# Kernel tuning notes

Measured on AMD Instinct MI355X. Metric: run time of the kernel, lower is better.

The kernel has to match this reference:

```python
import jax, jax.numpy as jnp
import numpy as np

N, E = 40000, 640000          # nodes, edges (avg degree 16)
IN_N, IN_E = 8 + 768, 2       # in_dim_node + in_dim_text, in_dim_edge
H, OUT, NC, L = 128, 128, 5, 2
EPS_BN, EPS_DEN = 1e-5, 1e-6


def setup_inputs() -> dict:
    key = jax.random.key(0)
    ks = jax.random.split(key, 16)
    w = lambda k, shape: jax.random.normal(k, shape, jnp.float32) * 0.05
    return {
        "node_feat": jax.random.normal(ks[0], (N, IN_N), jnp.float32),
        "edge_feat": jax.random.normal(ks[1], (E, IN_E), jnp.float32),
        "src": jax.random.randint(ks[2], (E,), 0, N),
        "dst": jax.random.randint(ks[3], (E,), 0, N),
        "enc_nw": w(ks[4], (IN_N, H)), "enc_nb": jnp.zeros((H,), jnp.float32),
        "enc_ew": w(ks[5], (IN_E, H)), "enc_eb": jnp.zeros((H,), jnp.float32),
        # per layer: 5 linears (order A, B, C, D, E)
        "lin_w": w(ks[6], (L, 5, H, H)), "lin_b": jnp.zeros((L, 5, H), jnp.float32),
        "bnh_g": jnp.ones((L, H), jnp.float32), "bnh_b": jnp.zeros((L, H), jnp.float32),
        "bne_g": jnp.ones((L, H), jnp.float32), "bne_b": jnp.zeros((L, H), jnp.float32),
        "mlp_w1": w(ks[7], (H, OUT)), "mlp_b1": jnp.zeros((OUT,), jnp.float32),
        "mlp_w2": w(ks[8], (OUT, NC)), "mlp_b2": jnp.zeros((NC,), jnp.float32),
    }


def _bn(x, g, b):
    # training-mode BatchNorm1d: batch stats, biased variance, eps=1e-5
    m = jnp.mean(x, axis=0)
    v = jnp.var(x, axis=0)
    return (x - m) * jax.lax.rsqrt(v + EPS_BN) * g + b


def reference(node_feat, edge_feat, src, dst, enc_nw, enc_nb, enc_ew, enc_eb,
              lin_w, lin_b, bnh_g, bnh_b, bne_g, bne_b,
              mlp_w1, mlp_b1, mlp_w2, mlp_b2):
    n = node_feat.shape[0]
    h = node_feat @ enc_nw + enc_nb          # [N, H]
    e = edge_feat @ enc_ew + enc_eb          # [E, H]
    for l in range(L):
        Ah = h @ lin_w[l, 0] + lin_b[l, 0]
        Bh = h @ lin_w[l, 1] + lin_b[l, 1]
        Ce = e @ lin_w[l, 2] + lin_b[l, 2]
        Dh = h @ lin_w[l, 3] + lin_b[l, 3]
        Eh = h @ lin_w[l, 4] + lin_b[l, 4]
        e_new = Ce + Dh[src] + Eh[dst]       # [E, H] edge gate logits
        sigma = jax.nn.sigmoid(e_new)
        num = jax.ops.segment_sum(sigma * Bh[src], dst, num_segments=n)
        den = jax.ops.segment_sum(sigma, dst, num_segments=n)
        h_new = Ah + num / (den + EPS_DEN)
        h = jax.nn.relu(_bn(h_new, bnh_g[l], bnh_b[l]))
        e = jax.nn.relu(_bn(e_new, bne_g[l], bne_b[l]))
    # MLP readout per node (dropout p=0 -> identity)
    logits = jax.nn.relu(h @ mlp_w1 + mlp_b1) @ mlp_w2 + mlp_b2
    return logits
```

## Files before the change

### kernel.cpp

```cpp
#include <hip/hip_runtime.h>
#include <math.h>

#define NN 40000
#define NE 640000
#define KIN 776
#define HH 128
#define NCLS 5

typedef __attribute__((ext_vector_type(8))) short bf16x8;
typedef __attribute__((ext_vector_type(4))) short bf16x4;
typedef __attribute__((ext_vector_type(4))) float f32x4;

__device__ __forceinline__ float bf2f(short u) {
    return __uint_as_float(((unsigned)(unsigned short)u) << 16);
}
__device__ __forceinline__ short f2bf(float f) {
    unsigned u = __float_as_uint(f);
    u += 0x7fffu + ((u >> 16) & 1u);
    return (short)(u >> 16);
}

enum { A_F32 = 0, A_BF16 = 1, A_BN = 2, A_BNF32 = 3 };

template<int AMODE, int NSTEP, bool TAIL8, bool GATHER, bool RELUOUT, bool CBF16>
__global__ __launch_bounds__(256)
void mfma_gemm(const float* __restrict__ Af, const short* __restrict__ Ab,
               const short* __restrict__ Wp, const float* __restrict__ bias,
               float* __restrict__ Cf, short* __restrict__ Cb,
               const float* __restrict__ bnp,
               const short* __restrict__ Dh, const short* __restrict__ Eh,
               const int* __restrict__ src, const int* __restrict__ dstv,
               int K)
{
    const int lane = threadIdx.x & 63;
    const int wave = threadIdx.x >> 6;
    const int q = lane >> 4;
    const int c16 = lane & 15;
    const int row = blockIdx.x * 64 + wave * 16 + c16;

    f32x4 acc[8];
#pragma unroll
    for (int n = 0; n < 8; ++n) acc[n] = (f32x4){0.f, 0.f, 0.f, 0.f};

    for (int kt = 0; kt < NSTEP; ++kt) {
        bf16x8 afrag;
        const int kbase = kt * 32 + q * 8;
        if (AMODE == A_BF16) {
            afrag = *(const bf16x8*)(Ab + (size_t)row * K + kbase);
        } else if (AMODE == A_F32) {
            if (!TAIL8 || kt < NSTEP - 1 || q == 0) {
                const float* p = Af + (size_t)row * K + kbase;
                const float4 x = *(const float4*)p;
                const float4 y = *(const float4*)(p + 4);
                afrag[0] = f2bf(x.x); afrag[1] = f2bf(x.y);
                afrag[2] = f2bf(x.z); afrag[3] = f2bf(x.w);
                afrag[4] = f2bf(y.x); afrag[5] = f2bf(y.y);
                afrag[6] = f2bf(y.z); afrag[7] = f2bf(y.w);
            } else {
#pragma unroll
                for (int j = 0; j < 8; ++j) afrag[j] = 0;
            }
        } else if (AMODE == A_BN) {
            const bf16x8 raw = *(const bf16x8*)(Ab + (size_t)row * K + kbase);
            const float4 s0 = *(const float4*)(bnp + kbase);
            const float4 s1 = *(const float4*)(bnp + kbase + 4);
            const float4 t0 = *(const float4*)(bnp + HH + kbase);
            const float4 t1 = *(const float4*)(bnp + HH + kbase + 4);
            const float scv[8] = {s0.x, s0.y, s0.z, s0.w, s1.x, s1.y, s1.z, s1.w};
            const float shv[8] = {t0.x, t0.y, t0.z, t0.w, t1.x, t1.y, t1.z, t1.w};
#pragma unroll
            for (int j = 0; j < 8; ++j)
                afrag[j] = f2bf(fmaxf(fmaf(bf2f(raw[j]), scv[j], shv[j]), 0.f));
        } else {
            const float* p = Af + (size_t)row * K + kbase;
            const float4 x = *(const float4*)p;
            const float4 y = *(const float4*)(p + 4);
            const float4 s0 = *(const float4*)(bnp + kbase);
            const float4 s1 = *(const float4*)(bnp + kbase + 4);
            const float4 t0 = *(const float4*)(bnp + HH + kbase);
            const float4 t1 = *(const float4*)(bnp + HH + kbase + 4);
            const float xv[8] = {x.x, x.y, x.z, x.w, y.x, y.y, y.z, y.w};
            const float scv[8] = {s0.x, s0.y, s0.z, s0.w, s1.x, s1.y, s1.z, s1.w};
            const float shv[8] = {t0.x, t0.y, t0.z, t0.w, t1.x, t1.y, t1.z, t1.w};
#pragma unroll
            for (int j = 0; j < 8; ++j)
                afrag[j] = f2bf(fmaxf(fmaf(xv[j], scv[j], shv[j]), 0.f));
        }
        const int kb = kt * 4 + q;
#pragma unroll
        for (int n = 0; n < 8; ++n) {
            const bf16x8 wfrag =
                *(const bf16x8*)(Wp + (size_t)kb * 1024 + (n * 16 + c16) * 8);
            acc[n] = __builtin_amdgcn_mfma_f32_16x16x32_bf16(wfrag, afrag, acc[n], 0, 0, 0);
        }
    }

    int sI = 0, dI = 0;
    if (GATHER) { sI = src[row]; dI = dstv[row]; }
#pragma unroll
    for (int n = 0; n < 8; ++n) {
        const int col = n * 16 + q * 4;
        const float4 b4 = *(const float4*)(bias + col);
        float v[4] = {acc[n][0] + b4.x, acc[n][1] + b4.y,
                      acc[n][2] + b4.z, acc[n][3] + b4.w};
        if (GATHER) {
            const bf16x4 dh = *(const bf16x4*)(Dh + (size_t)sI * HH + col);
            const bf16x4 eh = *(const bf16x4*)(Eh + (size_t)dI * HH + col);
#pragma unroll
            for (int j = 0; j < 4; ++j) v[j] += bf2f(dh[j]) + bf2f(eh[j]);
        }
        if (RELUOUT) {
#pragma unroll
            for (int j = 0; j < 4; ++j) v[j] = fmaxf(v[j], 0.f);
        }
        if (CBF16) {
            bf16x4 o;
#pragma unroll
            for (int j = 0; j < 4; ++j) o[j] = f2bf(v[j]);
            *(bf16x4*)(Cb + (size_t)row * HH + col) = o;
        } else {
            *(float4*)(Cf + (size_t)row * HH + col) = make_float4(v[0], v[1], v[2], v[3]);
        }
    }
}

template<bool ABN>
__global__ __launch_bounds__(256, 2)
void fused4_k(const short* __restrict__ hb, const float* __restrict__ hf,
              const float* __restrict__ bnp,
              const short* __restrict__ w0, const short* __restrict__ w1,
              const short* __restrict__ w2, const short* __restrict__ w3,
              const float* __restrict__ b0, const float* __restrict__ b1,
              const float* __restrict__ b2, const float* __restrict__ b3,
              float* __restrict__ Ah, short* __restrict__ Bh,
              short* __restrict__ Dh, short* __restrict__ Eh)
{
    const int lane = threadIdx.x & 63;
    const int wave = threadIdx.x >> 6;
    const int q = lane >> 4;
    const int c16 = lane & 15;
    const int row = blockIdx.x * 64 + wave * 16 + c16;

    f32x4 acc[4][8];
#pragma unroll
    for (int t = 0; t < 4; ++t)
#pragma unroll
        for (int n = 0; n < 8; ++n) acc[t][n] = (f32x4){0.f, 0.f, 0.f, 0.f};

    const short* const ws[4] = {w0, w1, w2, w3};
#pragma unroll
    for (int kt = 0; kt < 4; ++kt) {
        const int kbase = kt * 32 + q * 8;
        bf16x8 afrag;
        if (!ABN) {
            afrag = *(const bf16x8*)(hb + (size_t)row * HH + kbase);
        } else {
            const float* p = hf + (size_t)row * HH + kbase;
            const float4 x = *(const float4*)p;
            const float4 y = *(const float4*)(p + 4);
            const float4 s0 = *(const float4*)(bnp + kbase);
            const float4 s1 = *(const float4*)(bnp + kbase + 4);
            const float4 t0 = *(const float4*)(bnp + HH + kbase);
            const float4 t1 = *(const float4*)(bnp + HH + kbase + 4);
            const float xv[8] = {x.x, x.y, x.z, x.w, y.x, y.y, y.z, y.w};
            const float scv[8] = {s0.x, s0.y, s0.z, s0.w, s1.x, s1.y, s1.z, s1.w};
            const float shv[8] = {t0.x, t0.y, t0.z, t0.w, t1.x, t1.y, t1.z, t1.w};
#pragma unroll
            for (int j = 0; j < 8; ++j)
                afrag[j] = f2bf(fmaxf(fmaf(xv[j], scv[j], shv[j]), 0.f));
        }
        const int kb = kt * 4 + q;
#pragma unroll
        for (int t = 0; t < 4; ++t)
#pragma unroll
            for (int n = 0; n < 8; ++n) {
                const bf16x8 wfrag =
                    *(const bf16x8*)(ws[t] + (size_t)kb * 1024 + (n * 16 + c16) * 8);
                acc[t][n] = __builtin_amdgcn_mfma_f32_16x16x32_bf16(wfrag, afrag, acc[t][n], 0, 0, 0);
            }
    }

    const float* const bs[4] = {b0, b1, b2, b3};
#pragma unroll
    for (int t = 0; t < 4; ++t) {
#pragma unroll
        for (int n = 0; n < 8; ++n) {
            const int col = n * 16 + q * 4;
            const float4 b4 = *(const float4*)(bs[t] + col);
            const float v[4] = {acc[t][n][0] + b4.x, acc[t][n][1] + b4.y,
                                acc[t][n][2] + b4.z, acc[t][n][3] + b4.w};
            if (t == 0) {
                *(float4*)(Ah + (size_t)row * HH + col) = make_float4(v[0], v[1], v[2], v[3]);
            } else {
                bf16x4 o;
#pragma unroll
                for (int j = 0; j < 4; ++j) o[j] = f2bf(v[j]);
                short* dstp = (t == 1) ? Bh : ((t == 2) ? Dh : Eh);
                *(bf16x4*)(dstp + (size_t)row * HH + col) = o;
            }
        }
    }
}

__global__ __launch_bounds__(256)
void prepack_k(const float* __restrict__ enc_nw, const float* __restrict__ lin_w,
               const float* __restrict__ mlp_w1, short* __restrict__ wp)
{
    const int t = blockIdx.x * 256 + threadIdx.x;
    if (t >= 260 * 128) return;
    const int kbg = t >> 7, col = t & 127;
    const int kb0[11]  = {0, 100, 116, 132, 148, 164, 180, 196, 212, 228, 244};
    const int psel[11] = {0, 1, 1, 1, 1, 1, 1, 1, 1, 1, 2};
    const int soff[11] = {0, 0 * 16384, 1 * 16384, 3 * 16384, 4 * 16384,
                          5 * 16384, 6 * 16384, 7 * 16384, 8 * 16384, 9 * 16384, 0};
    const int Ksrc[11] = {KIN, 128, 128, 128, 128, 128, 128, 128, 128, 128, 128};
    int e = 10;
    while (e > 0 && kbg < kb0[e]) --e;
    const float* base = (psel[e] == 0) ? enc_nw : ((psel[e] == 1) ? lin_w : mlp_w1);
    const int kbl = kbg - kb0[e];
    bf16x8 o;
#pragma unroll
    for (int j = 0; j < 8; ++j) {
        const int k = kbl * 8 + j;
        const float v = (k < Ksrc[e]) ? base[(size_t)soff[e] + (size_t)k * HH + col] : 0.f;
        o[j] = f2bf(v);
    }
    *(bf16x8*)(wp + (size_t)kbg * 1024 + col * 8) = o;
}

__global__ void gpre_k(const float* __restrict__ enc_ew, const float* __restrict__ enc_eb,
                       const float* __restrict__ Wc, const float* __restrict__ bc,
                       float* __restrict__ G)
{
    const int c = threadIdx.x;
    float a0 = 0.f, a1 = 0.f, ab = 0.f;
    for (int k = 0; k < HH; ++k) {
        const float w = Wc[k * HH + c];
        a0 = fmaf(enc_ew[k], w, a0);
        a1 = fmaf(enc_ew[HH + k], w, a1);
        ab = fmaf(enc_eb[k], w, ab);
    }
    G[c] = a0; G[HH + c] = a1; G[2 * HH + c] = ab + bc[c];
}

__global__ __launch_bounds__(256)
void edge1_k(const float* __restrict__ ef, const int* __restrict__ eidx,
             const int* __restrict__ src_s, const int* __restrict__ dst_s,
             const float* __restrict__ G,
             const short* __restrict__ Dh, const short* __restrict__ Eh,
             short* __restrict__ enew, float* __restrict__ pbuf)
{
    const int tid = threadIdx.x;
    const int er = tid >> 4, cg = tid & 15;
    const int col = cg * 8;
    const float4 g00 = *(const float4*)(G + col);
    const float4 g01 = *(const float4*)(G + col + 4);
    const float4 g10 = *(const float4*)(G + HH + col);
    const float4 g11 = *(const float4*)(G + HH + col + 4);
    const float4 gb0 = *(const float4*)(G + 2 * HH + col);
    const float4 gb1 = *(const float4*)(G + 2 * HH + col + 4);
    const float G0v[8] = {g00.x, g00.y, g00.z, g00.w, g01.x, g01.y, g01.z, g01.w};
    const float G1v[8] = {g10.x, g10.y, g10.z, g10.w, g11.x, g11.y, g11.z, g11.w};
    const float GBv[8] = {gb0.x, gb0.y, gb0.z, gb0.w, gb1.x, gb1.y, gb1.z, gb1.w};
    float sa[8] = {}, qa[8] = {};
    for (int it = 0; it < 16; ++it) {
        const int i = blockIdx.x * 256 + it * 16 + er;
        const int e = eidx[i];
        const float f0 = ef[(size_t)e * 2];
        const float f1 = ef[(size_t)e * 2 + 1];
        const int s = src_s[i], d = dst_s[i];
        const bf16x8 dh = *(const bf16x8*)(Dh + (size_t)s * HH + col);
        const bf16x8 eh = *(const bf16x8*)(Eh + (size_t)d * HH + col);
        bf16x8 o;
#pragma unroll
        for (int j = 0; j < 8; ++j) {
            const float v = fmaf(f0, G0v[j], fmaf(f1, G1v[j], GBv[j]))
                            + bf2f(dh[j]) + bf2f(eh[j]);
            sa[j] += v; qa[j] += v * v;
            o[j] = f2bf(v);
        }
        *(bf16x8*)(enew + (size_t)i * HH + col) = o;
    }
    __shared__ float sred[16][136];
    const int slot = (blockIdx.x & 63) * 256;
#pragma unroll
    for (int j = 0; j < 8; ++j) sred[er][col + j] = sa[j];
    __syncthreads();
    for (int s2 = 8; s2 > 0; s2 >>= 1) {
        if (er < s2)
#pragma unroll
            for (int j = 0; j < 8; ++j) sred[er][col + j] += sred[er + s2][col + j];
        __syncthreads();
    }
    if (er == 0)
#pragma unroll
        for (int j = 0; j < 8; ++j) atomicAdd(pbuf + slot + col + j, sred[0][col + j]);
    __syncthreads();
#pragma unroll
    for (int j = 0; j < 8; ++j) sred[er][col + j] = qa[j];
    __syncthreads();
    for (int s2 = 8; s2 > 0; s2 >>= 1) {
        if (er < s2)
#pragma unroll
            for (int j = 0; j < 8; ++j) sred[er][col + j] += sred[er + s2][col + j];
        __syncthreads();
    }
    if (er == 0)
#pragma unroll
        for (int j = 0; j < 8; ++j) atomicAdd(pbuf + slot + 128 + col + j, sred[0][col + j]);
}

__global__ __launch_bounds__(256)
void hist_k(const int* __restrict__ dst, int* __restrict__ cnt)
{
    const int e = blockIdx.x * 256 + threadIdx.x;
    if (e < NE) atomicAdd(cnt + dst[e], 1);
}

__global__ __launch_bounds__(1024)
void scan_k(const int* __restrict__ cnt, int* __restrict__ rowptr, int* __restrict__ wr)
{
    __shared__ int s[1024];
    const int t = threadIdx.x;
    const int base = t * 40;
    int sum = 0;
    for (int i = 0; i < 40; ++i) {
        const int idx = base + i;
        if (idx < NN) sum += cnt[idx];
    }
    s[t] = sum;
    __syncthreads();
    for (int off = 1; off < 1024; off <<= 1) {
        const int v = (t >= off) ? s[t - off] : 0;
        __syncthreads();
        s[t] += v;
        __syncthreads();
    }
    int run = (t == 0) ? 0 : s[t - 1];
    for (int i = 0; i < 40; ++i) {
        const int idx = base + i;
        if (idx < NN) {
            rowptr[idx] = run;
            wr[idx] = run;
            run += cnt[idx];
        }
    }
    if (t == 1023) rowptr[NN] = s[1023];
}

__global__ __launch_bounds__(256)
void scatter_k2(const int* __restrict__ dst, const int* __restrict__ src,
                int* __restrict__ wr, int* __restrict__ eidx,
                int* __restrict__ src_s, int* __restrict__ dst_s)
{
    const int e = blockIdx.x * 256 + threadIdx.x;
    if (e < NE) {
        const int d = dst[e];
        const int p = atomicAdd(wr + d, 1);
        eidx[p] = e;
        src_s[p] = src[e];
        dst_s[p] = d;
    }
}

__global__ __launch_bounds__(128)
void seg_reduce8(const short* __restrict__ enew, const int* __restrict__ rowptr,
                 const int* __restrict__ src_s, const short* __restrict__ Bh,
                 const float* __restrict__ Ah, float* __restrict__ hnew,
                 float* __restrict__ pbuf)
{
    const int c = threadIdx.x;
    const int nb = blockIdx.x * 8;
    float sa = 0.f, qa = 0.f;
    for (int nn = 0; nn < 8; ++nn) {
        const int n = nb + nn;
        const int k0 = rowptr[n], k1 = rowptr[n + 1];
        float num = 0.f, den = 0.f;
        for (int k = k0; k < k1; ++k) {
            const float x = bf2f(enew[(size_t)k * HH + c]);
            const float sg = 1.f / (1.f + __expf(-x));
            const float bh = bf2f(Bh[(size_t)src_s[k] * HH + c]);
            den += sg;
            num = fmaf(sg, bh, num);
        }
        const size_t idx = (size_t)n * HH + c;
        const float x = Ah[idx] + num / (den + 1e-6f);
        hnew[idx] = x;
        sa += x; qa += x * x;
    }
    const int slot = (blockIdx.x & 63) * 256;
    atomicAdd(pbuf + slot + c, sa);
    atomicAdd(pbuf + slot + 128 + c, qa);
}

__global__ void make_bnp2(const float* __restrict__ pbuf, const float* __restrict__ g,
                          const float* __restrict__ b, float cntInv,
                          float* __restrict__ out)
{
    const int c = threadIdx.x;
    float s = 0.f, q = 0.f;
    for (int i = 0; i < 64; ++i) {
        s += pbuf[i * 256 + c];
        q += pbuf[i * 256 + 128 + c];
    }
    const float m = s * cntInv;
    const float var = q * cntInv - m * m;
    const float rs = rsqrtf(var + 1e-5f);
    const float sc = g[c] * rs;
    out[c] = sc;
    out[128 + c] = b[c] - m * sc;
}

__global__ __launch_bounds__(256)
void readout2(const short* __restrict__ z, const float* __restrict__ w2,
              const float* __restrict__ b2, float* __restrict__ out)
{
    const int idx = blockIdx.x * 256 + threadIdx.x;
    if (idx >= NN * NCLS) return;
    const int n = idx / NCLS, j = idx - n * NCLS;
    float acc = b2[j];
    const short* zr = z + (size_t)n * HH;
    for (int kk = 0; kk < 16; ++kk) {
        const bf16x8 zv = *(const bf16x8*)(zr + kk * 8);
#pragma unroll
        for (int j8 = 0; j8 < 8; ++j8)
            acc = fmaf(bf2f(zv[j8]), w2[(kk * 8 + j8) * NCLS + j], acc);
    }
    out[idx] = acc;
}

extern "C" void kernel_launch(void* const* d_in, const int* in_sizes, int n_in,
                              void* d_out, int out_size, void* d_ws, size_t ws_size,
                              hipStream_t stream)
{
    const float* node_feat = (const float*)d_in[0];
    const float* edge_feat = (const float*)d_in[1];
    const int*   src       = (const int*)d_in[2];
    const int*   dst       = (const int*)d_in[3];
    const float* enc_nw    = (const float*)d_in[4];
    const float* enc_nb    = (const float*)d_in[5];
    const float* enc_ew    = (const float*)d_in[6];
    const float* enc_eb    = (const float*)d_in[7];
    const float* lin_w     = (const float*)d_in[8];
    const float* lin_b     = (const float*)d_in[9];
    const float* bnh_g     = (const float*)d_in[10];
    const float* bnh_b     = (const float*)d_in[11];
    const float* bne_g     = (const float*)d_in[12];
    const float* bne_b     = (const float*)d_in[13];
    const float* mlp_w1    = (const float*)d_in[14];
    const float* mlp_b1    = (const float*)d_in[15];
    const float* mlp_w2    = (const float*)d_in[16];
    const float* mlp_b2    = (const float*)d_in[17];
    float* out = (float*)d_out;

    char* base = (char*)d_ws;
    size_t off = 0;
    auto alloc = [&](size_t bytes) -> void* {
        void* p = base + off;
        off = (off + bytes + 255) & ~(size_t)255;
        return p;
    };
    const size_t NH = (size_t)NN * HH;
    float* hnew  = (float*)alloc(NH * 4);
    float* Ah    = (float*)alloc(NH * 4);
    short* h0    = (short*)alloc(NH * 2);
    short* Bh    = (short*)alloc(NH * 2);
    short* Dh    = (short*)alloc(NH * 2);
    short* Eh    = (short*)alloc(NH * 2);
    short* z     = (short*)alloc(NH * 2);
    short* enew  = (short*)alloc((size_t)NE * HH * 2);
    short* wpack = (short*)alloc((size_t)260 * 1024 * 2);
    float* G     = (float*)alloc(384 * 4);
    float* bnpe  = (float*)alloc(256 * 4);
    float* bnph  = (float*)alloc(256 * 4);
    float* pbe   = (float*)alloc(16384 * 4);
    float* pbh0  = (float*)alloc(16384 * 4);
    float* pbh1  = (float*)alloc(16384 * 4);
    int* cnt     = (int*)alloc(NN * 4);
    int* rowptr  = (int*)alloc((NN + 1) * 4);
    int* wr      = (int*)alloc(NN * 4);
    int* eidx    = (int*)alloc((size_t)NE * 4);
    int* src_s   = (int*)alloc((size_t)NE * 4);
    int* dst_s   = (int*)alloc((size_t)NE * 4);

    const dim3 blk(256);

    hipMemsetAsync(cnt, 0, NN * 4, stream);
    hipMemsetAsync(pbe, 0, 3 * 16384 * 4, stream);
    hist_k<<<2500, blk, 0, stream>>>(dst, cnt);
    scan_k<<<1, 1024, 0, stream>>>(cnt, rowptr, wr);
    scatter_k2<<<2500, blk, 0, stream>>>(dst, src, wr, eidx, src_s, dst_s);
    prepack_k<<<130, blk, 0, stream>>>(enc_nw, lin_w, mlp_w1, wpack);
    gpre_k<<<1, 128, 0, stream>>>(enc_ew, enc_eb, lin_w + 2 * 16384, lin_b + 2 * HH, G);

    mfma_gemm<A_F32, 25, true, false, false, true><<<625, blk, 0, stream>>>(
        node_feat, nullptr, wpack, enc_nb, nullptr, h0,
        nullptr, nullptr, nullptr, nullptr, nullptr, KIN);

    {
        const float* Bv = lin_b;
        fused4_k<false><<<625, blk, 0, stream>>>(
            h0, nullptr, nullptr,
            wpack + (size_t)100 * 1024, wpack + (size_t)116 * 1024,
            wpack + (size_t)132 * 1024, wpack + (size_t)148 * 1024,
            Bv + 0 * HH, Bv + 1 * HH, Bv + 3 * HH, Bv + 4 * HH,
            Ah, Bh, Dh, Eh);
        edge1_k<<<2500, blk, 0, stream>>>(edge_feat, eidx, src_s, dst_s, G,
                                          Dh, Eh, enew, pbe);
        make_bnp2<<<1, 128, 0, stream>>>(pbe, bne_g, bne_b, 1.f / NE, bnpe);
        seg_reduce8<<<5000, 128, 0, stream>>>(enew, rowptr, src_s, Bh, Ah, hnew, pbh0);
        make_bnp2<<<1, 128, 0, stream>>>(pbh0, bnh_g, bnh_b, 1.f / NN, bnph);
    }

    {
        const float* Bv = lin_b + 5 * HH;
        fused4_k<true><<<625, blk, 0, stream>>>(
            nullptr, hnew, bnph,
            wpack + (size_t)164 * 1024, wpack + (size_t)180 * 1024,
            wpack + (size_t)212 * 1024, wpack + (size_t)228 * 1024,
            Bv + 0 * HH, Bv + 1 * HH, Bv + 3 * HH, Bv + 4 * HH,
            Ah, Bh, Dh, Eh);
        mfma_gemm<A_BN, 4, false, true, false, true><<<10000, blk, 0, stream>>>(
            nullptr, enew, wpack + (size_t)196 * 1024, Bv + 2 * HH,
            nullptr, enew, bnpe, Dh, Eh, src_s, dst_s, HH);
        seg_reduce8<<<5000, 128, 0, stream>>>(enew, rowptr, src_s, Bh, Ah, hnew, pbh1);
        make_bnp2<<<1, 128, 0, stream>>>(pbh1, bnh_g + HH, bnh_b + HH, 1.f / NN, bnph);
    }

    mfma_gemm<A_BNF32, 4, false, false, true, true><<<625, blk, 0, stream>>>(
        hnew, nullptr, wpack + (size_t)244 * 1024, mlp_b1, nullptr, z,
        bnph, nullptr, nullptr, nullptr, nullptr, HH);
    readout2<<<782, blk, 0, stream>>>(z, mlp_w2, mlp_b2, out);
}
```

Baseline: 881.6 us.

## Vectorize segment reduce, fuse MLP readout, and process two edge tiles per block

The per-node segment reduction is rewritten so that each wave handles one node with 16 lanes covering 8 columns each. Four edge slots run in parallel and are combined with cross-lane shuffles, using vectorized 16-byte loads of the edge gates and the gathered Bh rows. The second-layer edge GEMM becomes a dedicated kernel that processes 128 edge rows per block, reuses each weight fragment across two row tiles, and preloads the Dh/Eh gathers into the accumulators. The final MLP's first GEMM and the 5-class projection are fused into one kernel, removing the intermediate z buffer and a launch, at the cost of higher register pressure in the fused kernels.

```diff
diff --git a/kernel.cpp b/kernel.cpp
--- a/kernel.cpp
+++ b/kernel.cpp
@@ -20,17 +20,12 @@
     return (short)(u >> 16);
 }
 
-enum { A_F32 = 0, A_BF16 = 1, A_BN = 2, A_BNF32 = 3 };
-
-template<int AMODE, int NSTEP, bool TAIL8, bool GATHER, bool RELUOUT, bool CBF16>
-__global__ __launch_bounds__(256)
-void mfma_gemm(const float* __restrict__ Af, const short* __restrict__ Ab,
-               const short* __restrict__ Wp, const float* __restrict__ bias,
-               float* __restrict__ Cf, short* __restrict__ Cb,
-               const float* __restrict__ bnp,
-               const short* __restrict__ Dh, const short* __restrict__ Eh,
-               const int* __restrict__ src, const int* __restrict__ dstv,
-               int K)
+enum { A_F32 = 0 };
+
+template<int NSTEP, bool TAIL8>
+__global__ __launch_bounds__(256)
+void mfma_gemm(const float* __restrict__ Af, const short* __restrict__ Wp,
+               const float* __restrict__ bias, short* __restrict__ Cb, int K)
 {
     const int lane = threadIdx.x & 63;
     const int wave = threadIdx.x >> 6;
@@ -45,46 +40,17 @@
     for (int kt = 0; kt < NSTEP; ++kt) {
         bf16x8 afrag;
         const int kbase = kt * 32 + q * 8;
-        if (AMODE == A_BF16) {
-            afrag = *(const bf16x8*)(Ab + (size_t)row * K + kbase);
-        } else if (AMODE == A_F32) {
-            if (!TAIL8 || kt < NSTEP - 1 || q == 0) {
-                const float* p = Af + (size_t)row * K + kbase;
-                const float4 x = *(const float4*)p;
-                const float4 y = *(const float4*)(p + 4);
-                afrag[0] = f2bf(x.x); afrag[1] = f2bf(x.y);
-                afrag[2] = f2bf(x.z); afrag[3] = f2bf(x.w);
-                afrag[4] = f2bf(y.x); afrag[5] = f2bf(y.y);
-                afrag[6] = f2bf(y.z); afrag[7] = f2bf(y.w);
-            } else {
-#pragma unroll
-                for (int j = 0; j < 8; ++j) afrag[j] = 0;
-            }
-        } else if (AMODE == A_BN) {
-            const bf16x8 raw = *(const bf16x8*)(Ab + (size_t)row * K + kbase);
-            const float4 s0 = *(const float4*)(bnp + kbase);
-            const float4 s1 = *(const float4*)(bnp + kbase + 4);
-            const float4 t0 = *(const float4*)(bnp + HH + kbase);
-            const float4 t1 = *(const float4*)(bnp + HH + kbase + 4);
-            const float scv[8] = {s0.x, s0.y, s0.z, s0.w, s1.x, s1.y, s1.z, s1.w};
-            const float shv[8] = {t0.x, t0.y, t0.z, t0.w, t1.x, t1.y, t1.z, t1.w};
-#pragma unroll
-            for (int j = 0; j < 8; ++j)
-                afrag[j] = f2bf(fmaxf(fmaf(bf2f(raw[j]), scv[j], shv[j]), 0.f));
-        } else {
+        if (!TAIL8 || kt < NSTEP - 1 || q == 0) {
             const float* p = Af + (size_t)row * K + kbase;
             const float4 x = *(const float4*)p;
             const float4 y = *(const float4*)(p + 4);
-            const float4 s0 = *(const float4*)(bnp + kbase);
-            const float4 s1 = *(const float4*)(bnp + kbase + 4);
-            const float4 t0 = *(const float4*)(bnp + HH + kbase);
-            const float4 t1 = *(const float4*)(bnp + HH + kbase + 4);
-            const float xv[8] = {x.x, x.y, x.z, x.w, y.x, y.y, y.z, y.w};
-            const float scv[8] = {s0.x, s0.y, s0.z, s0.w, s1.x, s1.y, s1.z, s1.w};
-            const float shv[8] = {t0.x, t0.y, t0.z, t0.w, t1.x, t1.y, t1.z, t1.w};
-#pragma unroll
-            for (int j = 0; j < 8; ++j)
-                afrag[j] = f2bf(fmaxf(fmaf(xv[j], scv[j], shv[j]), 0.f));
+            afrag[0] = f2bf(x.x); afrag[1] = f2bf(x.y);
+            afrag[2] = f2bf(x.z); afrag[3] = f2bf(x.w);
+            afrag[4] = f2bf(y.x); afrag[5] = f2bf(y.y);
+            afrag[6] = f2bf(y.z); afrag[7] = f2bf(y.w);
+        } else {
+#pragma unroll
+            for (int j = 0; j < 8; ++j) afrag[j] = 0;
         }
         const int kb = kt * 4 + q;
 #pragma unroll
@@ -94,33 +60,88 @@
             acc[n] = __builtin_amdgcn_mfma_f32_16x16x32_bf16(wfrag, afrag, acc[n], 0, 0, 0);
         }
     }
-
-    int sI = 0, dI = 0;
-    if (GATHER) { sI = src[row]; dI = dstv[row]; }
 #pragma unroll
     for (int n = 0; n < 8; ++n) {
         const int col = n * 16 + q * 4;
         const float4 b4 = *(const float4*)(bias + col);
-        float v[4] = {acc[n][0] + b4.x, acc[n][1] + b4.y,
-                      acc[n][2] + b4.z, acc[n][3] + b4.w};
-        if (GATHER) {
-            const bf16x4 dh = *(const bf16x4*)(Dh + (size_t)sI * HH + col);
-            const bf16x4 eh = *(const bf16x4*)(Eh + (size_t)dI * HH + col);
-#pragma unroll
-            for (int j = 0; j < 4; ++j) v[j] += bf2f(dh[j]) + bf2f(eh[j]);
-        }
-        if (RELUOUT) {
-#pragma unroll
-            for (int j = 0; j < 4; ++j) v[j] = fmaxf(v[j], 0.f);
-        }
-        if (CBF16) {
-            bf16x4 o;
-#pragma unroll
-            for (int j = 0; j < 4; ++j) o[j] = f2bf(v[j]);
-            *(bf16x4*)(Cb + (size_t)row * HH + col) = o;
-        } else {
-            *(float4*)(Cf + (size_t)row * HH + col) = make_float4(v[0], v[1], v[2], v[3]);
-        }
+        bf16x4 o;
+        o[0] = f2bf(acc[n][0] + b4.x); o[1] = f2bf(acc[n][1] + b4.y);
+        o[2] = f2bf(acc[n][2] + b4.z); o[3] = f2bf(acc[n][3] + b4.w);
+        *(bf16x4*)(Cb + (size_t)row * HH + col) = o;
+    }
+}
+
+__global__ __launch_bounds__(256)
+void edge2_k(short* __restrict__ enew, const short* __restrict__ Wp,
+             const float* __restrict__ bias, const float* __restrict__ bnp,
+             const short* __restrict__ Dh, const short* __restrict__ Eh,
+             const int* __restrict__ src_s, const int* __restrict__ dst_s)
+{
+    const int lane = threadIdx.x & 63;
+    const int wave = threadIdx.x >> 6;
+    const int q = lane >> 4;
+    const int c16 = lane & 15;
+    const int row0 = blockIdx.x * 128 + wave * 16 + c16;
+    const int row1 = row0 + 64;
+
+    const int s0 = src_s[row0], d0 = dst_s[row0];
+    const int s1 = src_s[row1], d1 = dst_s[row1];
+
+    f32x4 acc[2][8];
+#pragma unroll
+    for (int n = 0; n < 8; ++n) {
+        const int col = n * 16 + q * 4;
+        const float4 b4 = *(const float4*)(bias + col);
+        const bf16x4 dh0 = *(const bf16x4*)(Dh + (size_t)s0 * HH + col);
+        const bf16x4 eh0 = *(const bf16x4*)(Eh + (size_t)d0 * HH + col);
+        const bf16x4 dh1 = *(const bf16x4*)(Dh + (size_t)s1 * HH + col);
+        const bf16x4 eh1 = *(const bf16x4*)(Eh + (size_t)d1 * HH + col);
+        const float bb[4] = {b4.x, b4.y, b4.z, b4.w};
+#pragma unroll
+        for (int j = 0; j < 4; ++j) {
+            acc[0][n][j] = bb[j] + bf2f(dh0[j]) + bf2f(eh0[j]);
+            acc[1][n][j] = bb[j] + bf2f(dh1[j]) + bf2f(eh1[j]);
+        }
+    }
+
+#pragma unroll
+    for (int kt = 0; kt < 4; ++kt) {
+        const int kbase = kt * 32 + q * 8;
+        const float4 sc0 = *(const float4*)(bnp + kbase);
+        const float4 sc1 = *(const float4*)(bnp + kbase + 4);
+        const float4 sh0 = *(const float4*)(bnp + HH + kbase);
+        const float4 sh1 = *(const float4*)(bnp + HH + kbase + 4);
+        const float scv[8] = {sc0.x, sc0.y, sc0.z, sc0.w, sc1.x, sc1.y, sc1.z, sc1.w};
+        const float shv[8] = {sh0.x, sh0.y, sh0.z, sh0.w, sh1.x, sh1.y, sh1.z, sh1.w};
+        const bf16x8 r0 = *(const bf16x8*)(enew + (size_t)row0 * HH + kbase);
+        const bf16x8 r1 = *(const bf16x8*)(enew + (size_t)row1 * HH + kbase);
+        bf16x8 a0, a1;
+#pragma unroll
+        for (int j = 0; j < 8; ++j) {
+            a0[j] = f2bf(fmaxf(fmaf(bf2f(r0[j]), scv[j], shv[j]), 0.f));
+            a1[j] = f2bf(fmaxf(fmaf(bf2f(r1[j]), scv[j], shv[j]), 0.f));
+        }
+        const int kb = kt * 4 + q;
+#pragma unroll
+        for (int n = 0; n < 8; ++n) {
+            const bf16x8 wfrag =
+                *(const bf16x8*)(Wp + (size_t)kb * 1024 + (n * 16 + c16) * 8);
+            acc[0][n] = __builtin_amdgcn_mfma_f32_16x16x32_bf16(wfrag, a0, acc[0][n], 0, 0, 0);
+            acc[1][n] = __builtin_amdgcn_mfma_f32_16x16x32_bf16(wfrag, a1, acc[1][n], 0, 0, 0);
+        }
+    }
+
+#pragma unroll
+    for (int n = 0; n < 8; ++n) {
+        const int col = n * 16 + q * 4;
+        bf16x4 o0, o1;
+#pragma unroll
+        for (int j = 0; j < 4; ++j) {
+            o0[j] = f2bf(acc[0][n][j]);
+            o1[j] = f2bf(acc[1][n][j]);
+        }
+        *(bf16x4*)(enew + (size_t)row0 * HH + col) = o0;
+        *(bf16x4*)(enew + (size_t)row1 * HH + col) = o1;
     }
 }
 
@@ -199,6 +220,74 @@
                 *(bf16x4*)(dstp + (size_t)row * HH + col) = o;
             }
         }
+    }
+}
+
+__global__ __launch_bounds__(256)
+void readout_k(const float* __restrict__ hnew, const float* __restrict__ bnp,
+               const short* __restrict__ Wp, const float* __restrict__ b1,
+               const float* __restrict__ w2, const float* __restrict__ b2,
+               float* __restrict__ out)
+{
+    const int lane = threadIdx.x & 63;
+    const int wave = threadIdx.x >> 6;
+    const int q = lane >> 4;
+    const int c16 = lane & 15;
+    const int row = blockIdx.x * 64 + wave * 16 + c16;
+
+    f32x4 acc[8];
+#pragma unroll
+    for (int n = 0; n < 8; ++n) acc[n] = (f32x4){0.f, 0.f, 0.f, 0.f};
+
+#pragma unroll
+    for (int kt = 0; kt < 4; ++kt) {
+        const int kbase = kt * 32 + q * 8;
+        const float* p = hnew + (size_t)row * HH + kbase;
+        const float4 x = *(const float4*)p;
+        const float4 y = *(const float4*)(p + 4);
+        const float4 s0 = *(const float4*)(bnp + kbase);
+        const float4 s1 = *(const float4*)(bnp + kbase + 4);
+        const float4 t0 = *(const float4*)(bnp + HH + kbase);
+        const float4 t1 = *(const float4*)(bnp + HH + kbase + 4);
+        const float xv[8] = {x.x, x.y, x.z, x.w, y.x, y.y, y.z, y.w};
+        const float scv[8] = {s0.x, s0.y, s0.z, s0.w, s1.x, s1.y, s1.z, s1.w};
+        const float shv[8] = {t0.x, t0.y, t0.z, t0.w, t1.x, t1.y, t1.z, t1.w};
+        bf16x8 afrag;
+#pragma unroll
+        for (int j = 0; j < 8; ++j)
+            afrag[j] = f2bf(fmaxf(fmaf(xv[j], scv[j], shv[j]), 0.f));
+        const int kb = kt * 4 + q;
+#pragma unroll
+        for (int n = 0; n < 8; ++n) {
+            const bf16x8 wfrag =
+                *(const bf16x8*)(Wp + (size_t)kb * 1024 + (n * 16 + c16) * 8);
+            acc[n] = __builtin_amdgcn_mfma_f32_16x16x32_bf16(wfrag, afrag, acc[n], 0, 0, 0);
+        }
+    }
+
+    float part[NCLS] = {};
+#pragma unroll
+    for (int n = 0; n < 8; ++n) {
+        const int col = n * 16 + q * 4;
+        const float4 b4 = *(const float4*)(b1 + col);
+        const float bb[4] = {b4.x, b4.y, b4.z, b4.w};
+#pragma unroll
+        for (int j = 0; j < 4; ++j) {
+            const float zv = fmaxf(acc[n][j] + bb[j], 0.f);
+#pragma unroll
+            for (int t = 0; t < NCLS; ++t)
+                part[t] = fmaf(zv, w2[(col + j) * NCLS + t], part[t]);
+        }
+    }
+#pragma unroll
+    for (int t = 0; t < NCLS; ++t) {
+        part[t] += __shfl_xor(part[t], 16, 64);
+        part[t] += __shfl_xor(part[t], 32, 64);
+    }
+    if (q == 0) {
+#pragma unroll
+        for (int t = 0; t < NCLS; ++t)
+            out[(size_t)row * NCLS + t] = part[t] + b2[t];
     }
 }
 
@@ -363,34 +452,64 @@
     }
 }
 
-__global__ __launch_bounds__(128)
-void seg_reduce8(const short* __restrict__ enew, const int* __restrict__ rowptr,
-                 const int* __restrict__ src_s, const short* __restrict__ Bh,
-                 const float* __restrict__ Ah, float* __restrict__ hnew,
-                 float* __restrict__ pbuf)
-{
-    const int c = threadIdx.x;
-    const int nb = blockIdx.x * 8;
-    float sa = 0.f, qa = 0.f;
+__global__ __launch_bounds__(256)
+void seg_reduce_v(const short* __restrict__ enew, const int* __restrict__ rowptr,
+                  const int* __restrict__ src_s, const short* __restrict__ Bh,
+                  const float* __restrict__ Ah, float* __restrict__ hnew,
+                  float* __restrict__ pbuf)
+{
+    const int wv = threadIdx.x >> 6;
+    const int lane = threadIdx.x & 63;
+    const int slot = lane >> 4;
+    const int cg = lane & 15;
+    const int col = cg * 8;
+    const int n0 = (blockIdx.x * 4 + wv) * 8;
+    float sa[8] = {}, qa[8] = {};
     for (int nn = 0; nn < 8; ++nn) {
-        const int n = nb + nn;
+        const int n = n0 + nn;
         const int k0 = rowptr[n], k1 = rowptr[n + 1];
-        float num = 0.f, den = 0.f;
-        for (int k = k0; k < k1; ++k) {
-            const float x = bf2f(enew[(size_t)k * HH + c]);
-            const float sg = 1.f / (1.f + __expf(-x));
-            const float bh = bf2f(Bh[(size_t)src_s[k] * HH + c]);
-            den += sg;
-            num = fmaf(sg, bh, num);
-        }
-        const size_t idx = (size_t)n * HH + c;
-        const float x = Ah[idx] + num / (den + 1e-6f);
-        hnew[idx] = x;
-        sa += x; qa += x * x;
-    }
-    const int slot = (blockIdx.x & 63) * 256;
-    atomicAdd(pbuf + slot + c, sa);
-    atomicAdd(pbuf + slot + 128 + c, qa);
+        float num[8] = {}, den[8] = {};
+        for (int k = k0 + slot; k < k1; k += 4) {
+            const bf16x8 ev = *(const bf16x8*)(enew + (size_t)k * HH + col);
+            const int s = src_s[k];
+            const bf16x8 bv = *(const bf16x8*)(Bh + (size_t)s * HH + col);
+#pragma unroll
+            for (int j = 0; j < 8; ++j) {
+                const float sg = 1.f / (1.f + __expf(-bf2f(ev[j])));
+                den[j] += sg;
+                num[j] = fmaf(sg, bf2f(bv[j]), num[j]);
+            }
+        }
+#pragma unroll
+        for (int j = 0; j < 8; ++j) {
+            num[j] += __shfl_xor(num[j], 16, 64);
+            den[j] += __shfl_xor(den[j], 16, 64);
+            num[j] += __shfl_xor(num[j], 32, 64);
+            den[j] += __shfl_xor(den[j], 32, 64);
+        }
+        if (slot == 0) {
+            const size_t idx = (size_t)n * HH + col;
+            const float4 a0 = *(const float4*)(Ah + idx);
+            const float4 a1 = *(const float4*)(Ah + idx + 4);
+            const float av[8] = {a0.x, a0.y, a0.z, a0.w, a1.x, a1.y, a1.z, a1.w};
+            float x[8];
+#pragma unroll
+            for (int j = 0; j < 8; ++j) {
+                x[j] = av[j] + num[j] / (den[j] + 1e-6f);
+                sa[j] += x[j]; qa[j] += x[j] * x[j];
+            }
+            *(float4*)(hnew + idx) = make_float4(x[0], x[1], x[2], x[3]);
+            *(float4*)(hnew + idx + 4) = make_float4(x[4], x[5], x[6], x[7]);
+        }
+    }
+    if (slot == 0) {
+        const int sl = (blockIdx.x & 63) * 256;
+#pragma unroll
+        for (int j = 0; j < 8; ++j) {
+            atomicAdd(pbuf + sl + col + j, sa[j]);
+            atomicAdd(pbuf + sl + 128 + col + j, qa[j]);
+        }
+    }
 }
 
 __global__ void make_bnp2(const float* __restrict__ pbuf, const float* __restrict__ g,
@@ -409,24 +528,6 @@
     const float sc = g[c] * rs;
     out[c] = sc;
     out[128 + c] = b[c] - m * sc;
-}
-
-__global__ __launch_bounds__(256)
-void readout2(const short* __restrict__ z, const float* __restrict__ w2,
-              const float* __restrict__ b2, float* __restrict__ out)
-{
-    const int idx = blockIdx.x * 256 + threadIdx.x;
-    if (idx >= NN * NCLS) return;
-    const int n = idx / NCLS, j = idx - n * NCLS;
-    float acc = b2[j];
-    const short* zr = z + (size_t)n * HH;
-    for (int kk = 0; kk < 16; ++kk) {
-        const bf16x8 zv = *(const bf16x8*)(zr + kk * 8);
-#pragma unroll
-        for (int j8 = 0; j8 < 8; ++j8)
-            acc = fmaf(bf2f(zv[j8]), w2[(kk * 8 + j8) * NCLS + j], acc);
-    }
-    out[idx] = acc;
 }
 
 extern "C" void kernel_launch(void* const* d_in, const int* in_sizes, int n_in,
@@ -467,7 +568,6 @@
     short* Bh    = (short*)alloc(NH * 2);
     short* Dh    = (short*)alloc(NH * 2);
     short* Eh    = (short*)alloc(NH * 2);
-    short* z     = (short*)alloc(NH * 2);
     short* enew  = (short*)alloc((size_t)NE * HH * 2);
     short* wpack = (short*)alloc((size_t)260 * 1024 * 2);
     float* G     = (float*)alloc(384 * 4);
@@ -493,9 +593,7 @@
     prepack_k<<<130, blk, 0, stream>>>(enc_nw, lin_w, mlp_w1, wpack);
     gpre_k<<<1, 128, 0, stream>>>(enc_ew, enc_eb, lin_w + 2 * 16384, lin_b + 2 * HH, G);
 
-    mfma_gemm<A_F32, 25, true, false, false, true><<<625, blk, 0, stream>>>(
-        node_feat, nullptr, wpack, enc_nb, nullptr, h0,
-        nullptr, nullptr, nullptr, nullptr, nullptr, KIN);
+    mfma_gemm<25, true><<<625, blk, 0, stream>>>(node_feat, wpack, enc_nb, h0, KIN);
 
     {
         const float* Bv = lin_b;
@@ -508,7 +606,7 @@
         edge1_k<<<2500, blk, 0, stream>>>(edge_feat, eidx, src_s, dst_s, G,
                                           Dh, Eh, enew, pbe);
         make_bnp2<<<1, 128, 0, stream>>>(pbe, bne_g, bne_b, 1.f / NE, bnpe);
-        seg_reduce8<<<5000, 128, 0, stream>>>(enew, rowptr, src_s, Bh, Ah, hnew, pbh0);
+        seg_reduce_v<<<1250, blk, 0, stream>>>(enew, rowptr, src_s, Bh, Ah, hnew, pbh0);
         make_bnp2<<<1, 128, 0, stream>>>(pbh0, bnh_g, bnh_b, 1.f / NN, bnph);
     }
 
@@ -520,15 +618,12 @@
             wpack + (size_t)212 * 1024, wpack + (size_t)228 * 1024,
             Bv + 0 * HH, Bv + 1 * HH, Bv + 3 * HH, Bv + 4 * HH,
             Ah, Bh, Dh, Eh);
-        mfma_gemm<A_BN, 4, false, true, false, true><<<10000, blk, 0, stream>>>(
-            nullptr, enew, wpack + (size_t)196 * 1024, Bv + 2 * HH,
-            nullptr, enew, bnpe, Dh, Eh, src_s, dst_s, HH);
-        seg_reduce8<<<5000, 128, 0, stream>>>(enew, rowptr, src_s, Bh, Ah, hnew, pbh1);
+        edge2_k<<<5000, blk, 0, stream>>>(enew, wpack + (size_t)196 * 1024,
+                                          Bv + 2 * HH, bnpe, Dh, Eh, src_s, dst_s);
+        seg_reduce_v<<<1250, blk, 0, stream>>>(enew, rowptr, src_s, Bh, Ah, hnew, pbh1);
         make_bnp2<<<1, 128, 0, stream>>>(pbh1, bnh_g + HH, bnh_b + HH, 1.f / NN, bnph);
     }
 
-    mfma_gemm<A_BNF32, 4, false, false, true, true><<<625, blk, 0, stream>>>(
-        hnew, nullptr, wpack + (size_t)244 * 1024, mlp_b1, nullptr, z,
-        bnph, nullptr, nullptr, nullptr, nullptr, HH);
-    readout2<<<782, blk, 0, stream>>>(z, mlp_w2, mlp_b2, out);
-}
+    readout_k<<<625, blk, 0, stream>>>(hnew, bnph, wpack + (size_t)244 * 1024,
+                                       mlp_b1, mlp_w2, mlp_b2, out);
+}
```

Result: faster. 816.0 us (-7.4%).
